# Kernel optimization log

Hardware: AMD Instinct MI355X
Metric: run time of the kernel (lower is better)

Reference implementation:

```python
import jax, jax.numpy as jnp
import numpy as np
from jax import lax

INP_MODES = (4, 8, 8, 4)
OUT_MODES = (4, 8, 8, 4)
RANKS = (1, 8, 8, 8, 1)  # mat_ranks
WINDOW = (3, 3)


def setup_inputs() -> dict:
    key = jax.random.key(0)
    ks = jax.random.split(key, 7)
    d = {}
    d["x"] = jax.random.normal(ks[0], (16, 32, 32, 1024), jnp.float32)
    # conv filter: [kh, kw, 1, r0]
    d["filters"] = jax.random.normal(ks[1], (WINDOW[0], WINDOW[1], 1, RANKS[0]), jnp.float32) * (1.0 / 3.0)
    # TT cores: core_i has shape [m_i * r_{i+1}, r_i * n_i]
    for i in range(4):
        shp = (OUT_MODES[i] * RANKS[i + 1], RANKS[i] * INP_MODES[i])
        d[f"core{i}"] = jax.random.normal(ks[2 + i], shp, jnp.float32) * (1.0 / np.sqrt(shp[1]).astype(np.float32))
    d["bias"] = jnp.zeros((int(np.prod(OUT_MODES)),), jnp.float32)
    return d


def tt_conv(x, filters, cores, bias):
    B, H, W, C = x.shape  # C == prod(INP_MODES)
    r0 = filters.shape[3]
    # depthwise-style: every channel of every batch item becomes its own 1-channel map
    tmp = x.transpose(0, 3, 1, 2).reshape(B * C, H, W, 1)
    tmp = lax.conv_general_dilated(tmp, filters, window_strides=(1, 1), padding="SAME",
                                   dimension_numbers=("NHWC", "HWIO", "NHWC"))
    h, w = tmp.shape[1], tmp.shape[2]
    # [B, C, h, w, r0] -> [r0, C, B, h, w]
    tmp = tmp.reshape(B, C, h, w, r0).transpose(4, 1, 0, 2, 3)
    # chained TT-core contractions (fixed small loop over num_dim)
    for i in range(len(cores)):
        tmp = tmp.reshape(RANKS[i] * INP_MODES[i], -1)
        tmp = cores[i] @ tmp                      # [m_i * r_{i+1}, rest]
        tmp = tmp.reshape(OUT_MODES[i], -1).T     # move m_i to the back
    M = int(np.prod(OUT_MODES))
    out = tmp.reshape(-1, h, w, M) + bias
    return jax.nn.relu(out)


def reference(x, filters, core0, core1, core2, core3, bias):
    return tt_conv(x, filters, [core0, core1, core2, core3], bias)
```

## Files before the change

### kernel.cpp

```cpp
#include <hip/hip_runtime.h>
#include <hip/hip_bf16.h>
#include <stdint.h>

typedef __attribute__((ext_vector_type(8))) short short8;
typedef __attribute__((ext_vector_type(4))) float f32x4;

__device__ inline unsigned short f2bf(float f) {
  union { float f; unsigned u; } v; v.f = f;
  unsigned r = v.u + 0x7fffu + ((v.u >> 16) & 1u);
  return (unsigned short)(r >> 16);
}

__global__ __launch_bounds__(256) void tt_build_T(
    const float* __restrict__ c0, const float* __restrict__ c1,
    const float* __restrict__ c2, const float* __restrict__ c3,
    unsigned short* __restrict__ Tb) {
  __shared__ float L[8192];
  __shared__ float R[8192];
  int t = threadIdx.x;
  for (int i = t; i < 8192; i += 256) {
    int n1 = i & 7, n0 = (i >> 3) & 3, r2 = (i >> 5) & 7, m1 = (i >> 8) & 7, m0 = i >> 11;
    float s = 0.f;
#pragma unroll
    for (int r1 = 0; r1 < 8; ++r1)
      s += c0[(m0 * 8 + r1) * 4 + n0] * c1[(m1 * 8 + r2) * 64 + r1 * 8 + n1];
    L[i] = s;
  }
  for (int i = t; i < 8192; i += 256) {
    int n3 = i & 3, n2 = (i >> 2) & 7, m3 = (i >> 5) & 3, m2 = (i >> 7) & 7, r2 = i >> 10;
    float s = 0.f;
#pragma unroll
    for (int r3 = 0; r3 < 8; ++r3)
      s += c2[(m2 * 8 + r3) * 64 + r2 * 8 + n2] * c3[m3 * 32 + r3 * 4 + n3];
    R[i] = s;
  }
  __syncthreads();
  int base = blockIdx.x * 4096;
  for (int j = 0; j < 16; ++j) {
    int lin = j * 256 + t;
    int g = base + lin;
    int m = g >> 10, n = g & 1023;
    int m0 = m >> 8, m1 = (m >> 5) & 7, m2 = (m >> 2) & 7, m3 = m & 3;
    int n0 = n >> 8, n1 = (n >> 5) & 7, n2 = (n >> 2) & 7, n3 = n & 3;
    float s = 0.f;
#pragma unroll
    for (int r2 = 0; r2 < 8; ++r2)
      s += L[(((m0 * 8 + m1) * 8 + r2) * 4 + n0) * 8 + n1] *
           R[(((r2 * 8 + m2) * 4 + m3) * 8 + n2) * 4 + n3];
    Tb[(size_t)m * 1024 + n] = f2bf(s);
  }
}

__global__ __launch_bounds__(256) void tt_conv3x3_lds(
    const float* __restrict__ x, const float* __restrict__ filt,
    unsigned short* __restrict__ D) {
  __shared__ float xs[10][32][32];
  int bid = blockIdx.x;
  int cg = bid & 31, strip = (bid >> 5) & 3, b = bid >> 7;
  int h0 = strip * 8;
  int tid = threadIdx.x;
  float4 z4; z4.x = z4.y = z4.z = z4.w = 0.f;
#pragma unroll
  for (int i = 0; i < 10; ++i) {
    int j = tid + 256 * i;
    int row = j >> 8, w = (j >> 3) & 31, c4 = j & 7;
    int gh = h0 - 1 + row;
    float4 v = z4;
    if ((unsigned)gh < 32u)
      v = *reinterpret_cast<const float4*>(x + ((size_t)((b * 32 + gh) * 32 + w)) * 1024 + cg * 32 + c4 * 4);
    *reinterpret_cast<float4*>(&xs[row][w][c4 * 4]) = v;
  }
  float F[9];
#pragma unroll
  for (int i = 0; i < 9; ++i) F[i] = filt[i];
  __syncthreads();

  int c4 = tid & 7, w = tid >> 3;
#define LD3(r, d0, d1, d2) { \
    d1 = *reinterpret_cast<const float4*>(&xs[r][w][c4 * 4]); \
    d0 = (w > 0)  ? *reinterpret_cast<const float4*>(&xs[r][w - 1][c4 * 4]) : z4; \
    d2 = (w < 31) ? *reinterpret_cast<const float4*>(&xs[r][w + 1][c4 * 4]) : z4; }
#define ACC4(a, f, v) { a.x += (f) * v.x; a.y += (f) * v.y; a.z += (f) * v.z; a.w += (f) * v.w; }
  float4 a00, a01, a02, a10, a11, a12, a20, a21, a22;
  LD3(0, a00, a01, a02);
  LD3(1, a10, a11, a12);
#pragma unroll
  for (int h = 0; h < 8; ++h) {
    LD3(h + 2, a20, a21, a22);
    float4 s = z4;
    ACC4(s, F[0], a00); ACC4(s, F[1], a01); ACC4(s, F[2], a02);
    ACC4(s, F[3], a10); ACC4(s, F[4], a11); ACC4(s, F[5], a12);
    ACC4(s, F[6], a20); ACC4(s, F[7], a21); ACC4(s, F[8], a22);
    ushort4 o;
    o.x = f2bf(s.x); o.y = f2bf(s.y); o.z = f2bf(s.z); o.w = f2bf(s.w);
    *reinterpret_cast<ushort4*>(&D[((size_t)(b * 1024 + (h0 + h) * 32 + w)) * 1024 + cg * 32 + c4 * 4]) = o;
    a00 = a10; a01 = a11; a02 = a12;
    a10 = a20; a11 = a21; a12 = a22;
  }
#undef LD3
#undef ACC4
}

__device__ inline void stage16(const unsigned short* g, unsigned short* l) {
  __builtin_amdgcn_global_load_lds(
      (const __attribute__((address_space(1))) void*)g,
      (__attribute__((address_space(3))) void*)l, 16, 0, 0);
}

__global__ __launch_bounds__(512, 2) void tt_gemm_8p(
    const unsigned short* __restrict__ A,
    const unsigned short* __restrict__ Bt,
    const float* __restrict__ bias,
    float* __restrict__ C) {
  __shared__ unsigned short lds[2][2][16384];
  const int tid = threadIdx.x;
  const int lane = tid & 63, wave = tid >> 6;
  const int wr = wave >> 2, wc = wave & 3;
  const int lr = lane & 15, kc = lane >> 4;

  int lin = blockIdx.x + blockIdx.y * 64;
  int Lg = ((lin & 7) << 5) | (lin >> 3);
  int brow = (Lg & 63) * 256;
  int bcol = (Lg >> 6) * 256;

  int q8[4];
  const unsigned short* srcA[4];
  const unsigned short* srcB[4];
#pragma unroll
  for (int j = 0; j < 4; ++j) {
    int q = tid + 512 * j;
    int row = q >> 3, cp = q & 7, c = cp ^ (row & 7);
    q8[j] = q * 8;
    srcA[j] = A + (size_t)(brow + row) * 1024 + c * 8;
    srcB[j] = Bt + (size_t)(bcol + row) * 1024 + c * 8;
  }

  int offA[8][2], offB[4][2];
#pragma unroll
  for (int m = 0; m < 8; ++m) {
    int row = wr * 128 + m * 16 + lr;
#pragma unroll
    for (int ks = 0; ks < 2; ++ks) {
      int cp = (ks * 4 + kc) ^ (row & 7);
      offA[m][ks] = row * 64 + cp * 8;
    }
  }
#pragma unroll
  for (int n = 0; n < 4; ++n) {
    int row = wc * 64 + n * 16 + lr;
#pragma unroll
    for (int ks = 0; ks < 2; ++ks) {
      int cp = (ks * 4 + kc) ^ (row & 7);
      offB[n][ks] = row * 64 + cp * 8;
    }
  }

  f32x4 acc[8][4] = {};

#define SUBPHASE(RB, MH, KS, LOADB) { \
    short8 af[4]; \
    if (LOADB) { \
      _Pragma("unroll") for (int n = 0; n < 4; ++n) \
        bfr[n] = *reinterpret_cast<const short8*>(&lds[RB][1][offB[n][KS]]); \
    } \
    _Pragma("unroll") for (int m = 0; m < 4; ++m) \
      af[m] = *reinterpret_cast<const short8*>(&lds[RB][0][offA[(MH) * 4 + m][KS]]); \
    __builtin_amdgcn_s_barrier(); \
    asm volatile("s_waitcnt lgkmcnt(0)" ::: "memory"); \
    __builtin_amdgcn_sched_barrier(0); \
    __builtin_amdgcn_s_setprio(1); \
    _Pragma("unroll") for (int m = 0; m < 4; ++m) \
      _Pragma("unroll") for (int n = 0; n < 4; ++n) \
        acc[(MH) * 4 + m][n] = __builtin_amdgcn_mfma_f32_16x16x32_bf16(af[m], bfr[n], acc[(MH) * 4 + m][n], 0, 0, 0); \
    __builtin_amdgcn_s_setprio(0); \
    __builtin_amdgcn_sched_barrier(0); \
    __builtin_amdgcn_s_barrier(); \
  }

#define KITER(RB, SB, KT, DO_STAGE, VMS) { \
    if (DO_STAGE) { \
      _Pragma("unroll") for (int j = 0; j < 4; ++j) { \
        stage16(srcA[j] + (KT) * 64, &lds[SB][0][q8[j]]); \
        stage16(srcB[j] + (KT) * 64, &lds[SB][1][q8[j]]); \
      } \
    } \
    asm volatile("s_waitcnt vmcnt(" VMS ")" ::: "memory"); \
    __builtin_amdgcn_s_barrier(); \
    { short8 bfr[4]; \
      SUBPHASE(RB, 0, 0, 1) \
      SUBPHASE(RB, 1, 0, 0) \
      SUBPHASE(RB, 0, 1, 1) \
      SUBPHASE(RB, 1, 1, 0) } }

#pragma unroll
  for (int j = 0; j < 4; ++j) {
    stage16(srcA[j], &lds[0][0][q8[j]]);
    stage16(srcB[j], &lds[0][1][q8[j]]);
  }

  for (int t = 0; t < 14; t += 2) {
    KITER(0, 1, t + 1, 1, "8")
    KITER(1, 0, t + 2, 1, "8")
  }
  KITER(0, 1, 15, 1, "8")
  KITER(1, 0, 0, 0, "0")

#undef KITER
#undef SUBPHASE

#pragma unroll
  for (int n = 0; n < 4; ++n) {
    int col = bcol + wc * 64 + n * 16 + lr;
    float bv = bias[col];
#pragma unroll
    for (int m = 0; m < 8; ++m) {
#pragma unroll
      for (int j = 0; j < 4; ++j) {
        int row = brow + wr * 128 + m * 16 + kc * 4 + j;
        float v = acc[m][n][j] + bv;
        C[(size_t)row * 1024 + col] = v > 0.f ? v : 0.f;
      }
    }
  }
}

extern "C" void kernel_launch(void* const* d_in, const int* in_sizes, int n_in,
                              void* d_out, int out_size, void* d_ws, size_t ws_size,
                              hipStream_t stream) {
  const float* x = (const float*)d_in[0];
  const float* filt = (const float*)d_in[1];
  const float* c0 = (const float*)d_in[2];
  const float* c1 = (const float*)d_in[3];
  const float* c2 = (const float*)d_in[4];
  const float* c3 = (const float*)d_in[5];
  const float* bias = (const float*)d_in[6];
  float* out = (float*)d_out;

  unsigned short* Tb = (unsigned short*)d_ws;
  unsigned short* D = Tb + (size_t)1024 * 1024;

  tt_build_T<<<256, 256, 0, stream>>>(c0, c1, c2, c3, Tb);
  tt_conv3x3_lds<<<2048, 256, 0, stream>>>(x, filt, D);
  dim3 grid(64, 4);
  tt_gemm_8p<<<grid, 512, 0, stream>>>(D, Tb, bias, out);
}
```

Measured before the change: 82.42 us.

## Restructure GEMM into 3-stage K=32 LDS pipeline with float4 epilogue

Replaces the double-buffered K=64 tile GEMM with a triple-buffered K=32 pipeline that uses a new swizzled LDS layout packing two rows per 64-element line. B and A tiles are staged at separate points inside each k-tile so global-to-LDS copies overlap the MFMA work. MFMA operands are swapped so each lane holds four consecutive output columns, which lets the epilogue apply bias and ReLU and store with float4 writes instead of scalar stores. The smaller K step doubles the number of barriers and k-iterations, and the index and vmcnt bookkeeping becomes more intricate.

Measured after the change: 79.88 us. -3.1%, faster.

```diff
diff --git a/kernel.cpp b/kernel.cpp
--- a/kernel.cpp
+++ b/kernel.cpp
@@ -107,119 +107,113 @@
       (__attribute__((address_space(3))) void*)l, 16, 0, 0);
 }
 
-__global__ __launch_bounds__(512, 2) void tt_gemm_8p(
+__global__ __launch_bounds__(512, 2) void tt_gemm_p3(
     const unsigned short* __restrict__ A,
     const unsigned short* __restrict__ Bt,
     const float* __restrict__ bias,
     float* __restrict__ C) {
-  __shared__ unsigned short lds[2][2][16384];
+  __shared__ unsigned short lds[3][2][8192];
   const int tid = threadIdx.x;
   const int lane = tid & 63, wave = tid >> 6;
   const int wr = wave >> 2, wc = wave & 3;
   const int lr = lane & 15, kc = lane >> 4;
+  const int rg = kc;
 
   int lin = blockIdx.x + blockIdx.y * 64;
   int Lg = ((lin & 7) << 5) | (lin >> 3);
   int brow = (Lg & 63) * 256;
   int bcol = (Lg >> 6) * 256;
 
-  int q8[4];
-  const unsigned short* srcA[4];
-  const unsigned short* srcB[4];
-#pragma unroll
-  for (int j = 0; j < 4; ++j) {
-    int q = tid + 512 * j;
-    int row = q >> 3, cp = q & 7, c = cp ^ (row & 7);
-    q8[j] = q * 8;
-    srcA[j] = A + (size_t)(brow + row) * 1024 + c * 8;
-    srcB[j] = Bt + (size_t)(bcol + row) * 1024 + c * 8;
-  }
-
-  int offA[8][2], offB[4][2];
+  int rowq0, cq0, rowq1, cq1;
+  { int q = tid;       int li = q >> 3, sp = q & 7, sl = sp ^ (li & 7); rowq0 = 2 * li + (sl >> 2); cq0 = sl & 3; }
+  { int q = tid + 512; int li = q >> 3, sp = q & 7, sl = sp ^ (li & 7); rowq1 = 2 * li + (sl >> 2); cq1 = sl & 3; }
+  const unsigned short* srcA0 = A + (size_t)(brow + rowq0) * 1024 + cq0 * 8;
+  const unsigned short* srcA1 = A + (size_t)(brow + rowq1) * 1024 + cq1 * 8;
+  const unsigned short* srcB0 = Bt + (size_t)(bcol + rowq0) * 1024 + cq0 * 8;
+  const unsigned short* srcB1 = Bt + (size_t)(bcol + rowq1) * 1024 + cq1 * 8;
+  const int l0 = tid * 8, l1 = (tid + 512) * 8;
+
+  int offA[8], offB[4];
 #pragma unroll
   for (int m = 0; m < 8; ++m) {
     int row = wr * 128 + m * 16 + lr;
-#pragma unroll
-    for (int ks = 0; ks < 2; ++ks) {
-      int cp = (ks * 4 + kc) ^ (row & 7);
-      offA[m][ks] = row * 64 + cp * 8;
-    }
+    int li = row >> 1, sl = (row & 1) * 4 + kc;
+    offA[m] = (li * 8 + (sl ^ (li & 7))) * 8;
   }
 #pragma unroll
   for (int n = 0; n < 4; ++n) {
     int row = wc * 64 + n * 16 + lr;
-#pragma unroll
-    for (int ks = 0; ks < 2; ++ks) {
-      int cp = (ks * 4 + kc) ^ (row & 7);
-      offB[n][ks] = row * 64 + cp * 8;
-    }
+    int li = row >> 1, sl = (row & 1) * 4 + kc;
+    offB[n] = (li * 8 + (sl ^ (li & 7))) * 8;
   }
 
   f32x4 acc[8][4] = {};
 
-#define SUBPHASE(RB, MH, KS, LOADB) { \
-    short8 af[4]; \
-    if (LOADB) { \
-      _Pragma("unroll") for (int n = 0; n < 4; ++n) \
-        bfr[n] = *reinterpret_cast<const short8*>(&lds[RB][1][offB[n][KS]]); \
-    } \
-    _Pragma("unroll") for (int m = 0; m < 4; ++m) \
-      af[m] = *reinterpret_cast<const short8*>(&lds[RB][0][offA[(MH) * 4 + m][KS]]); \
-    __builtin_amdgcn_s_barrier(); \
-    asm volatile("s_waitcnt lgkmcnt(0)" ::: "memory"); \
-    __builtin_amdgcn_sched_barrier(0); \
-    __builtin_amdgcn_s_setprio(1); \
-    _Pragma("unroll") for (int m = 0; m < 4; ++m) \
-      _Pragma("unroll") for (int n = 0; n < 4; ++n) \
-        acc[(MH) * 4 + m][n] = __builtin_amdgcn_mfma_f32_16x16x32_bf16(af[m], bfr[n], acc[(MH) * 4 + m][n], 0, 0, 0); \
-    __builtin_amdgcn_s_setprio(0); \
-    __builtin_amdgcn_sched_barrier(0); \
-    __builtin_amdgcn_s_barrier(); \
-  }
-
-#define KITER(RB, SB, KT, DO_STAGE, VMS) { \
-    if (DO_STAGE) { \
-      _Pragma("unroll") for (int j = 0; j < 4; ++j) { \
-        stage16(srcA[j] + (KT) * 64, &lds[SB][0][q8[j]]); \
-        stage16(srcB[j] + (KT) * 64, &lds[SB][1][q8[j]]); \
-      } \
-    } \
+#define STAGE_B(S, T) { stage16(srcB0 + (T) * 32, &lds[S][1][l0]); \
+                        stage16(srcB1 + (T) * 32, &lds[S][1][l1]); }
+#define STAGE_A(S, T) { stage16(srcA0 + (T) * 32, &lds[S][0][l0]); \
+                        stage16(srcA1 + (T) * 32, &lds[S][0][l1]); }
+
+#define KTILE(RB, SB, T2, VMS) { \
+    short8 bfr[4]; \
+    if ((T2) >= 0) STAGE_B(SB, T2); \
     asm volatile("s_waitcnt vmcnt(" VMS ")" ::: "memory"); \
     __builtin_amdgcn_s_barrier(); \
-    { short8 bfr[4]; \
-      SUBPHASE(RB, 0, 0, 1) \
-      SUBPHASE(RB, 1, 0, 0) \
-      SUBPHASE(RB, 0, 1, 1) \
-      SUBPHASE(RB, 1, 1, 0) } }
-
-#pragma unroll
-  for (int j = 0; j < 4; ++j) {
-    stage16(srcA[j], &lds[0][0][q8[j]]);
-    stage16(srcB[j], &lds[0][1][q8[j]]);
-  }
-
-  for (int t = 0; t < 14; t += 2) {
-    KITER(0, 1, t + 1, 1, "8")
-    KITER(1, 0, t + 2, 1, "8")
-  }
-  KITER(0, 1, 15, 1, "8")
-  KITER(1, 0, 0, 0, "0")
-
-#undef KITER
-#undef SUBPHASE
+    { short8 af[4]; \
+      _Pragma("unroll") for (int m = 0; m < 4; ++m) \
+        af[m] = *reinterpret_cast<const short8*>(&lds[RB][0][offA[m]]); \
+      _Pragma("unroll") for (int n = 0; n < 4; ++n) \
+        bfr[n] = *reinterpret_cast<const short8*>(&lds[RB][1][offB[n]]); \
+      asm volatile("s_waitcnt lgkmcnt(0)"); \
+      __builtin_amdgcn_s_setprio(1); \
+      _Pragma("unroll") for (int m = 0; m < 4; ++m) \
+        _Pragma("unroll") for (int n = 0; n < 4; ++n) \
+          acc[m][n] = __builtin_amdgcn_mfma_f32_16x16x32_bf16(bfr[n], af[m], acc[m][n], 0, 0, 0); \
+      __builtin_amdgcn_s_setprio(0); } \
+    __builtin_amdgcn_s_barrier(); \
+    if ((T2) >= 0) STAGE_A(SB, T2); \
+    __builtin_amdgcn_s_barrier(); \
+    { short8 af[4]; \
+      _Pragma("unroll") for (int m = 0; m < 4; ++m) \
+        af[m] = *reinterpret_cast<const short8*>(&lds[RB][0][offA[4 + m]]); \
+      asm volatile("s_waitcnt lgkmcnt(0)"); \
+      __builtin_amdgcn_s_setprio(1); \
+      _Pragma("unroll") for (int m = 0; m < 4; ++m) \
+        _Pragma("unroll") for (int n = 0; n < 4; ++n) \
+          acc[4 + m][n] = __builtin_amdgcn_mfma_f32_16x16x32_bf16(bfr[n], af[m], acc[4 + m][n], 0, 0, 0); \
+      __builtin_amdgcn_s_setprio(0); } \
+    __builtin_amdgcn_s_barrier(); }
+
+  STAGE_B(0, 0); STAGE_A(0, 0);
+  STAGE_B(1, 1); STAGE_A(1, 1);
+
+  for (int t = 0; t < 30; t += 3) {
+    KTILE(0, 2, t + 2, "6")
+    KTILE(1, 0, t + 3, "6")
+    KTILE(2, 1, t + 4, "6")
+  }
+  KTILE(0, 0, -1, "4")
+  KTILE(1, 1, -1, "0")
+
+#undef KTILE
+#undef STAGE_A
+#undef STAGE_B
 
 #pragma unroll
   for (int n = 0; n < 4; ++n) {
-    int col = bcol + wc * 64 + n * 16 + lr;
-    float bv = bias[col];
+    int col = bcol + wc * 64 + n * 16 + rg * 4;
+    float4 bv = *reinterpret_cast<const float4*>(&bias[col]);
 #pragma unroll
     for (int m = 0; m < 8; ++m) {
-#pragma unroll
-      for (int j = 0; j < 4; ++j) {
-        int row = brow + wr * 128 + m * 16 + kc * 4 + j;
-        float v = acc[m][n][j] + bv;
-        C[(size_t)row * 1024 + col] = v > 0.f ? v : 0.f;
-      }
+      int row = brow + wr * 128 + m * 16 + lr;
+      f32x4 v = acc[m][n];
+      float4 o;
+      o.x = v[0] + bv.x; o.y = v[1] + bv.y; o.z = v[2] + bv.z; o.w = v[3] + bv.w;
+      o.x = o.x > 0.f ? o.x : 0.f;
+      o.y = o.y > 0.f ? o.y : 0.f;
+      o.z = o.z > 0.f ? o.z : 0.f;
+      o.w = o.w > 0.f ? o.w : 0.f;
+      *reinterpret_cast<float4*>(&C[(size_t)row * 1024 + col]) = o;
     }
   }
 }
@@ -242,5 +236,5 @@
   tt_build_T<<<256, 256, 0, stream>>>(c0, c1, c2, c3, Tb);
   tt_conv3x3_lds<<<2048, 256, 0, stream>>>(x, filt, D);
   dim3 grid(64, 4);
-  tt_gemm_8p<<<grid, 512, 0, stream>>>(D, Tb, bias, out);
-}
+  tt_gemm_p3<<<grid, 512, 0, stream>>>(D, Tb, bias, out);
+}
```
